# Kernel optimization log

Hardware: AMD Instinct MI355X
Metric: run time of the kernel (lower is better)

The kernel has to match this reference:

```python
import jax, jax.numpy as jnp
import numpy as np

B, T, H, W, C = 2, 8, 32, 32, 192
DI, N, K, DTR = 384, 16, 4, 12   # d_inner=2*dim, d_state, scan directions, dt_rank=ceil(dim/16)
LT, HID = 77, 768
L = T * H * W


def setup_inputs() -> dict:
    key = jax.random.key(0)
    ks = jax.random.split(key, 16)
    r = lambda i, shape, s=1.0: jax.random.normal(ks[i], shape, dtype=jnp.float32) * s
    return {
        "x": r(0, (B, T, H, W, C)),
        "text": r(1, (B, LT, C)),
        "cpe1_w": r(2, (C, 1, 3, 3, 3), 0.05), "cpe1_b": jnp.zeros((C,), jnp.float32),
        "cpe2_w": r(3, (C, 1, 3, 3, 3), 0.05), "cpe2_b": jnp.zeros((C,), jnp.float32),
        "norm1_g": jnp.ones((C,), jnp.float32), "norm1_b": jnp.zeros((C,), jnp.float32),
        "norm2_g": jnp.ones((C,), jnp.float32), "norm2_b": jnp.zeros((C,), jnp.float32),
        "in_proj_w": r(4, (2 * DI, C), 0.02), "in_proj_b": jnp.zeros((2 * DI,), jnp.float32),
        "text_proj_w": r(5, (DI, C), 0.02), "text_proj_b": jnp.zeros((DI,), jnp.float32),
        "conv_w": r(6, (DI, 1, 3, 3, 3), 0.05), "conv_b": jnp.zeros((DI,), jnp.float32),
        "x_proj_w": r(7, (K, DTR + 2 * N, DI), 0.02),
        "dt_proj_w": r(8, (K, DI, DTR), 0.1), "dt_proj_b": r(9, (K, DI), 0.1),
        "A_log": jnp.log(jnp.tile(jnp.arange(1.0, N + 1.0, dtype=jnp.float32)[None, None, :], (K, DI, 1))),
        "Ds": jnp.ones((K, DI), jnp.float32),
        "out_norm_g": jnp.ones((DI,), jnp.float32), "out_norm_b": jnp.zeros((DI,), jnp.float32),
        "out_proj_w": r(10, (C, DI), 0.02),
        "fc1_w": r(11, (HID, C), 0.02), "fc1_b": jnp.zeros((HID,), jnp.float32),
        "fc2_w": r(12, (C, HID), 0.02), "fc2_b": jnp.zeros((C,), jnp.float32),
    }


def _ln(x, g, b, eps=1e-6):
    m = x.mean(-1, keepdims=True)
    v = jnp.mean((x - m) ** 2, -1, keepdims=True)
    return (x - m) * jax.lax.rsqrt(v + eps) * g + b


def _dwconv3d(x, w, b):  # x [B, Ch, T, H, W], depthwise 3x3x3, SAME padding
    y = jax.lax.conv_general_dilated(x, w, (1, 1, 1), 'SAME',
                                     feature_group_count=x.shape[1],
                                     dimension_numbers=('NCDHW', 'OIDHW', 'NCDHW'))
    return y + b[None, :, None, None, None]


def _cpe(x, w, b):  # conv positional encoding, channels-last in/out
    return jnp.transpose(_dwconv3d(jnp.transpose(x, (0, 4, 1, 2, 3)), w, b), (0, 2, 3, 4, 1))


def _ss2d(x, text, p):
    # in-projection -> (x, z) gate split
    xz = x @ p['in_proj_w'].T + p['in_proj_b']           # [B,T,H,W,2*DI]
    xi, z = jnp.split(xz, 2, axis=-1)
    # text conditioning (pooled text tokens -> channel bias)
    cond = jax.nn.silu(text.mean(1) @ p['text_proj_w'].T + p['text_proj_b'])  # [B,DI]
    xi = xi + cond[:, None, None, None, :]
    # depthwise conv3d + SiLU
    xc = jax.nn.silu(_dwconv3d(jnp.transpose(xi, (0, 4, 1, 2, 3)), p['conv_w'], p['conv_b']))  # [B,DI,T,H,W]
    # cross-scan: (t,h,w), (t,w,h) and their reversals
    x0 = xc.reshape(B, DI, L)
    x1 = jnp.swapaxes(xc, 3, 4).reshape(B, DI, L)
    xs = jnp.stack([x0, x1, jnp.flip(x0, -1), jnp.flip(x1, -1)], 1)  # [B,K,DI,L]
    # per-direction projections
    xdbl = jnp.einsum('bkdl,kcd->bkcl', xs, p['x_proj_w'])
    dtr, Bm, Cm = jnp.split(xdbl, [DTR, DTR + N], axis=2)            # [B,K,DTR,L],[B,K,N,L],[B,K,N,L]
    dt = jax.nn.softplus(jnp.einsum('bkrl,kdr->bkdl', dtr, p['dt_proj_w']) + p['dt_proj_b'][None, :, :, None])
    A = -jnp.exp(p['A_log'])                                          # [K,DI,N]
    def step(h, inp):
        u_l, dt_l, B_l, C_l = inp
        h = h * jnp.exp(dt_l[..., None] * A) + (dt_l * u_l)[..., None] * B_l[:, :, None, :]
        return h, jnp.einsum('bkdn,bkn->bkd', h, C_l)
    seq = (xs.transpose(3, 0, 1, 2), dt.transpose(3, 0, 1, 2),
           Bm.transpose(3, 0, 1, 2), Cm.transpose(3, 0, 1, 2))
    _, ys = jax.lax.scan(step, jnp.zeros((B, K, DI, N), xs.dtype), seq)  # ys [L,B,K,DI]
    ys = ys.transpose(1, 2, 3, 0) + p['Ds'][None, :, :, None] * xs       # [B,K,DI,L]
    # merge the 4 directions back into (t,h,w) order
    unt = lambda y: jnp.swapaxes(y.reshape(B, DI, T, W, H), 3, 4).reshape(B, DI, L)
    y = ys[:, 0] + jnp.flip(ys[:, 2], -1) + unt(ys[:, 1]) + unt(jnp.flip(ys[:, 3], -1))
    y = _ln(y.transpose(0, 2, 1), p['out_norm_g'], p['out_norm_b']).reshape(B, T, H, W, DI)
    y = y * jax.nn.silu(z)
    return y @ p['out_proj_w'].T


def reference(x, text, cpe1_w, cpe1_b, cpe2_w, cpe2_b, norm1_g, norm1_b, norm2_g, norm2_b,
              in_proj_w, in_proj_b, text_proj_w, text_proj_b, conv_w, conv_b,
              x_proj_w, dt_proj_w, dt_proj_b, A_log, Ds, out_norm_g, out_norm_b, out_proj_w,
              fc1_w, fc1_b, fc2_w, fc2_b):
    p = dict(in_proj_w=in_proj_w, in_proj_b=in_proj_b, text_proj_w=text_proj_w,
             text_proj_b=text_proj_b, conv_w=conv_w, conv_b=conv_b, x_proj_w=x_proj_w,
             dt_proj_w=dt_proj_w, dt_proj_b=dt_proj_b, A_log=A_log, Ds=Ds,
             out_norm_g=out_norm_g, out_norm_b=out_norm_b, out_proj_w=out_proj_w)
    x = x + _cpe(x, cpe1_w, cpe1_b)
    x = x + _ss2d(_ln(x, norm1_g, norm1_b), text, p)
    x = x + _cpe(x, cpe2_w, cpe2_b)
    h = _ln(x, norm2_g, norm2_b)
    x = x + (jax.nn.gelu(h @ fc1_w.T + fc1_b) @ fc2_w.T + fc2_b)
    return x
```

## Files before the change

### kernel.cpp

```cpp
#include <hip/hip_runtime.h>
#include <hip/hip_bf16.h>

#define DEV __device__ __forceinline__

namespace {

constexpr int cB = 2, cT = 8, cH = 32, cW = 32, cC = 192;
constexpr int cDI = 384, cN = 16, cK = 4, cDTR = 12, cLT = 77, cHID = 768;
constexpr int cL  = cT * cH * cW;
constexpr int cBL = cB * cL;
constexpr int SEG = 128, SEGLEN = cL / SEG;
constexpr int XROW = cDTR + 2 * cN;
constexpr int XSTR = 48;

typedef __attribute__((ext_vector_type(8))) short bf16x8;
typedef __attribute__((ext_vector_type(4))) float f32x4;
typedef __attribute__((ext_vector_type(2))) float f32x2;
typedef __attribute__((ext_vector_type(4))) short short4v;

DEV float bfu2f(unsigned short u) { return __uint_as_float(((unsigned)u) << 16); }
DEV float ldsel(const void* p, size_t i, int f32) {
  return f32 ? ((const float*)p)[i] : bfu2f(((const unsigned short*)p)[i]);
}
template <int F32>
DEV float4 ld4(const void* p, size_t e) {
  if (F32) return *(const float4*)((const float*)p + e);
  ushort4 u = *(const ushort4*)((const unsigned short*)p + e);
  return make_float4(bfu2f(u.x), bfu2f(u.y), bfu2f(u.z), bfu2f(u.w));
}
DEV short f2bf(float f) {
  unsigned u = __float_as_uint(f);
  u += 0x7fffu + ((u >> 16) & 1u);
  return (short)(u >> 16);
}
DEV float siluf(float x) { return x / (1.f + __expf(-x)); }
DEV float softplusf(float x) { return (x > 20.f) ? x : __logf(1.f + __expf(x)); }
DEV float gelut(float x) {
  float u = 0.7978845608028654f * (x + 0.044715f * x * x * x);
  float e = __expf(2.f * u);
  float th = 1.f - 2.f / (e + 1.f);
  return 0.5f * x * (1.f + th);
}
DEV f32x2 mk2(float a, float b) { f32x2 v; v[0] = a; v[1] = b; return v; }

__global__ void __launch_bounds__(256) detect_kernel(
    const unsigned short* __restrict__ xa, const unsigned short* __restrict__ wp,
    int* __restrict__ flg) {
  __shared__ int cnt[2];
  if (threadIdx.x < 2) cnt[threadIdx.x] = 0;
  __syncthreads();
  int l0 = 0, l1 = 0;
  for (int i = threadIdx.x; i < 1024; i += 256) {
    float v = bfu2f(xa[2 * i]); float a = fabsf(v);
    if (v == 0.f || (a > 1e-8f && a < 1e4f)) l0++;
    float u = bfu2f(wp[2 * i]); float bq = fabsf(u);
    if (u == 0.f || (bq > 1e-8f && bq < 1e4f)) l1++;
  }
  atomicAdd(&cnt[0], l0); atomicAdd(&cnt[1], l1);
  __syncthreads();
  if (threadIdx.x == 0) {
    flg[0] = (cnt[0] < 614) ? 1 : 0;
    flg[1] = (cnt[1] < 614) ? 1 : 0;
    flg[2] = 1;
  }
}

__global__ void __launch_bounds__(256) prep_kernel(
    const void* __restrict__ cvw, const void* __restrict__ cvb,
    const void* __restrict__ c1w, const void* __restrict__ c1b,
    const void* __restrict__ c2w, const void* __restrict__ c2b,
    const int* __restrict__ flg,
    float* __restrict__ wcv, float* __restrict__ bcv,
    float* __restrict__ w1, float* __restrict__ b1,
    float* __restrict__ w2, float* __restrict__ b2) {
  int pf = flg[1];
  int i = blockIdx.x * 256 + threadIdx.x;
  int r = i;
  if (r < 27 * cDI) { int j = r / cDI, d = r % cDI; wcv[r] = ldsel(cvw, (size_t)d * 27 + j, pf); return; }
  r -= 27 * cDI;
  if (r < cDI) { bcv[r] = ldsel(cvb, r, pf); return; }
  r -= cDI;
  if (r < 27 * cC) { int j = r / cC, c = r % cC; w1[r] = ldsel(c1w, (size_t)c * 27 + j, pf); return; }
  r -= 27 * cC;
  if (r < cC) { b1[r] = ldsel(c1b, r, pf); return; }
  r -= cC;
  if (r < 27 * cC) { int j = r / cC, c = r % cC; w2[r] = ldsel(c2w, (size_t)c * 27 + j, pf); return; }
  r -= 27 * cC;
  if (r < cC) { b2[r] = ldsel(c2b, r, pf); return; }
}

template <int F32>
DEV void cpe_body(const void* __restrict__ xin, const float* __restrict__ wT,
                  const float* __restrict__ bs, int idx, float* __restrict__ out) {
  int c = (idx % (cC / 4)) * 4; int pv = idx / (cC / 4);
  int w0 = (pv & 15) << 1;
  int rest = pv >> 4;
  int h = rest & 31; int bt = rest >> 5; int t = bt & 7; int b = bt >> 3;
  float4 bias = *(const float4*)(bs + c);
  float4 acc0 = bias, acc1 = bias;
  const float4 zero = make_float4(0.f, 0.f, 0.f, 0.f);
#pragma unroll
  for (int dz = 0; dz < 3; ++dz) {
    int tt = t + dz - 1; if ((unsigned)tt >= (unsigned)cT) continue;
#pragma unroll
    for (int dy = 0; dy < 3; ++dy) {
      int hh = h + dy - 1; if ((unsigned)hh >= (unsigned)cH) continue;
      int base = (tt << 10) + (hh << 5);
      const float* wr = wT + (dz * 9 + dy * 3) * cC + c;
      float4 wv0 = *(const float4*)(wr);
      float4 wv1 = *(const float4*)(wr + cC);
      float4 wv2 = *(const float4*)(wr + 2 * cC);
      size_t rb = ((size_t)b * cL + base) * cC + c;
      float4 xm1 = (w0 > 0)  ? ld4<F32>(xin, rb + (size_t)(w0 - 1) * cC) : zero;
      float4 x0v = ld4<F32>(xin, rb + (size_t)w0 * cC);
      float4 x1v = ld4<F32>(xin, rb + (size_t)(w0 + 1) * cC);
      float4 x2v = (w0 < 30) ? ld4<F32>(xin, rb + (size_t)(w0 + 2) * cC) : zero;
      acc0.x += wv0.x*xm1.x + wv1.x*x0v.x + wv2.x*x1v.x;
      acc0.y += wv0.y*xm1.y + wv1.y*x0v.y + wv2.y*x1v.y;
      acc0.z += wv0.z*xm1.z + wv1.z*x0v.z + wv2.z*x1v.z;
      acc0.w += wv0.w*xm1.w + wv1.w*x0v.w + wv2.w*x1v.w;
      acc1.x += wv0.x*x0v.x + wv1.x*x1v.x + wv2.x*x2v.x;
      acc1.y += wv0.y*x0v.y + wv1.y*x1v.y + wv2.y*x2v.y;
      acc1.z += wv0.z*x0v.z + wv1.z*x1v.z + wv2.z*x2v.z;
      acc1.w += wv0.w*x0v.w + wv1.w*x1v.w + wv2.w*x2v.w;
    }
  }
  size_t bv0 = (size_t)b * cL + (t << 10) + (h << 5) + w0;
  float4 r0 = ld4<F32>(xin, bv0 * cC + c);
  float4 r1 = ld4<F32>(xin, (bv0 + 1) * cC + c);
  *(float4*)(out + bv0 * cC + c) =
      make_float4(r0.x + acc0.x, r0.y + acc0.y, r0.z + acc0.z, r0.w + acc0.w);
  *(float4*)(out + (bv0 + 1) * cC + c) =
      make_float4(r1.x + acc1.x, r1.y + acc1.y, r1.z + acc1.z, r1.w + acc1.w);
}

__global__ void __launch_bounds__(256) cpe_kernel(
    const void* __restrict__ xin, const float* __restrict__ wT,
    const float* __restrict__ bs, const int* __restrict__ flg, int afidx,
    float* __restrict__ out) {
  int idx = blockIdx.x * 256 + threadIdx.x;
  if (idx >= cBL * cC / 8) return;
  if (flg[afidx]) cpe_body<1>(xin, wT, bs, idx, out);
  else            cpe_body<0>(xin, wT, bs, idx, out);
}

__global__ void __launch_bounds__(256) dwconv_silu_kernel(
    const unsigned short* __restrict__ xin, const float* __restrict__ wT,
    const float* __restrict__ bs, unsigned short* __restrict__ out) {
  int idx = blockIdx.x * 256 + threadIdx.x;
  if (idx >= cBL * cDI / 8) return;
  int d = (idx % (cDI / 4)) * 4; int pv = idx / (cDI / 4);
  int w0 = (pv & 15) << 1;
  int rest = pv >> 4;
  int h = rest & 31; int bt = rest >> 5; int t = bt & 7; int b = bt >> 3;
  float4 bias = *(const float4*)(bs + d);
  float4 acc0 = bias, acc1 = bias;
  const float4 zero = make_float4(0.f, 0.f, 0.f, 0.f);
#pragma unroll
  for (int dz = 0; dz < 3; ++dz) {
    int tt = t + dz - 1; if ((unsigned)tt >= (unsigned)cT) continue;
#pragma unroll
    for (int dy = 0; dy < 3; ++dy) {
      int hh = h + dy - 1; if ((unsigned)hh >= (unsigned)cH) continue;
      int base = (tt << 10) + (hh << 5);
      const float* wr = wT + (dz * 9 + dy * 3) * cDI + d;
      float4 wv0 = *(const float4*)(wr);
      float4 wv1 = *(const float4*)(wr + cDI);
      float4 wv2 = *(const float4*)(wr + 2 * cDI);
      size_t rb = ((size_t)b * cL + base) * cDI + d;
      float4 xm1 = (w0 > 0)  ? ld4<0>(xin, rb + (size_t)(w0 - 1) * cDI) : zero;
      float4 x0v = ld4<0>(xin, rb + (size_t)w0 * cDI);
      float4 x1v = ld4<0>(xin, rb + (size_t)(w0 + 1) * cDI);
      float4 x2v = (w0 < 30) ? ld4<0>(xin, rb + (size_t)(w0 + 2) * cDI) : zero;
      acc0.x += wv0.x*xm1.x + wv1.x*x0v.x + wv2.x*x1v.x;
      acc0.y += wv0.y*xm1.y + wv1.y*x0v.y + wv2.y*x1v.y;
      acc0.z += wv0.z*xm1.z + wv1.z*x0v.z + wv2.z*x1v.z;
      acc0.w += wv0.w*xm1.w + wv1.w*x0v.w + wv2.w*x1v.w;
      acc1.x += wv0.x*x0v.x + wv1.x*x1v.x + wv2.x*x2v.x;
      acc1.y += wv0.y*x0v.y + wv1.y*x1v.y + wv2.y*x2v.y;
      acc1.z += wv0.z*x0v.z + wv1.z*x1v.z + wv2.z*x2v.z;
      acc1.w += wv0.w*x0v.w + wv1.w*x1v.w + wv2.w*x2v.w;
    }
  }
  size_t bv0 = (size_t)b * cL + (t << 10) + (h << 5) + w0;
  ushort4 o0, o1;
  o0.x = (unsigned short)f2bf(siluf(acc0.x));
  o0.y = (unsigned short)f2bf(siluf(acc0.y));
  o0.z = (unsigned short)f2bf(siluf(acc0.z));
  o0.w = (unsigned short)f2bf(siluf(acc0.w));
  o1.x = (unsigned short)f2bf(siluf(acc1.x));
  o1.y = (unsigned short)f2bf(siluf(acc1.y));
  o1.z = (unsigned short)f2bf(siluf(acc1.z));
  o1.w = (unsigned short)f2bf(siluf(acc1.w));
  *(ushort4*)(out + bv0 * cDI + d) = o0;
  *(ushort4*)(out + (bv0 + 1) * cDI + d) = o1;
}

__global__ void __launch_bounds__(256) lnb_kernel(
    const float* __restrict__ in, const void* __restrict__ g,
    const void* __restrict__ bb, const int* __restrict__ flg,
    unsigned short* __restrict__ out) {
  int pf = flg[1];
  int row = blockIdx.x * 4 + (threadIdx.x >> 6);
  int lane = threadIdx.x & 63;
  const float* x = in + (size_t)row * cC;
  float v0 = x[lane], v1 = x[lane + 64], v2 = x[lane + 128];
  float s1 = v0 + v1 + v2;
  float s2 = v0 * v0 + v1 * v1 + v2 * v2;
#pragma unroll
  for (int off = 32; off > 0; off >>= 1) {
    s1 += __shfl_xor(s1, off);
    s2 += __shfl_xor(s2, off);
  }
  float mean = s1 * (1.f / cC);
  float var = s2 * (1.f / cC) - mean * mean;
  float rstd = rsqrtf(var + 1e-6f);
  unsigned short* o = out + (size_t)row * cC;
  o[lane]       = (unsigned short)f2bf((v0 - mean) * rstd * ldsel(g, lane, pf)       + ldsel(bb, lane, pf));
  o[lane + 64]  = (unsigned short)f2bf((v1 - mean) * rstd * ldsel(g, lane + 64, pf)  + ldsel(bb, lane + 64, pf));
  o[lane + 128] = (unsigned short)f2bf((v2 - mean) * rstd * ldsel(g, lane + 128, pf) + ldsel(bb, lane + 128, pf));
}

__global__ void __launch_bounds__(384) text_cond_kernel(
    const void* __restrict__ text, const void* __restrict__ tw,
    const void* __restrict__ tb, const int* __restrict__ flg,
    float* __restrict__ cond) {
  int af = flg[0], pf = flg[1];
  __shared__ float mean[cC];
  int b = blockIdx.x;
  for (int c = threadIdx.x; c < cC; c += 384) {
    float s = 0.f;
    for (int t = 0; t < cLT; ++t) s += ldsel(text, ((size_t)b * cLT + t) * cC + c, af);
    mean[c] = s * (1.f / cLT);
  }
  __syncthreads();
  int di = threadIdx.x;
  float a = ldsel(tb, di, pf);
  for (int c = 0; c < cC; ++c) a += mean[c] * ldsel(tw, di * cC + c, pf);
  cond[b * cDI + di] = siluf(a);
}

template <int MODE>
__global__ void __launch_bounds__(256) gemm_mfma_kernel(
    const void* __restrict__ A, const void* __restrict__ W,
    int N, int K, const void* __restrict__ bias, const int* __restrict__ flg,
    const float* __restrict__ extra, float* __restrict__ out,
    unsigned short* __restrict__ out2) {
  constexpr int BM = 128, BN = 64, BK = 64, PK = 72;
  __shared__ short As[BM * PK];
  __shared__ short Bs[BN * PK];
  int pf = flg[1];
  int tid = threadIdx.x;
  int m0 = blockIdx.y * BM, n0 = blockIdx.x * BN;
  int lane = tid & 63, wv = tid >> 6;
  int wm = (wv >> 1) * 64, wn = (wv & 1) * 32;
  int lr = lane & 15, quad = lane >> 4;
  f32x4 acc[4][2];
#pragma unroll
  for (int mi = 0; mi < 4; ++mi)
#pragma unroll
    for (int ni = 0; ni < 2; ++ni) { acc[mi][ni][0]=0.f; acc[mi][ni][1]=0.f; acc[mi][ni][2]=0.f; acc[mi][ni][3]=0.f; }
  int ar = tid >> 1, aks = (tid & 1) * 32;
  int wr = tid >> 2, wks = (tid & 3) * 16;
  for (int k0 = 0; k0 < K; k0 += BK) {
    {
      const unsigned short* ap = (const unsigned short*)A + (size_t)(m0 + ar) * K + k0 + aks;
      short* da = &As[ar * PK + aks];
#pragma unroll
      for (int i = 0; i < 4; ++i)
        *(bf16x8*)(da + i * 8) = *(const bf16x8*)(ap + i * 8);
    }
    {
      int nr = n0 + wr;
      short* db = &Bs[wr * PK + wks];
      if (nr < N) {
        size_t wi = (size_t)nr * K + k0 + wks;
        if (pf) {
          float4 wv0 = *(const float4*)((const float*)W + wi);
          float4 wv1 = *(const float4*)((const float*)W + wi + 4);
          float4 wv2 = *(const float4*)((const float*)W + wi + 8);
          float4 wv3 = *(const float4*)((const float*)W + wi + 12);
          short4v h0, h1, h2, h3;
          h0.x = f2bf(wv0.x); h0.y = f2bf(wv0.y); h0.z = f2bf(wv0.z); h0.w = f2bf(wv0.w);
          h1.x = f2bf(wv1.x); h1.y = f2bf(wv1.y); h1.z = f2bf(wv1.z); h1.w = f2bf(wv1.w);
          h2.x = f2bf(wv2.x); h2.y = f2bf(wv2.y); h2.z = f2bf(wv2.z); h2.w = f2bf(wv2.w);
          h3.x = f2bf(wv3.x); h3.y = f2bf(wv3.y); h3.z = f2bf(wv3.z); h3.w = f2bf(wv3.w);
          *(short4v*)(db) = h0;
          *(short4v*)(db + 4) = h1;
          *(short4v*)(db + 8) = h2;
          *(short4v*)(db + 12) = h3;
        } else {
          *(bf16x8*)(db) = *(const bf16x8*)((const unsigned short*)W + wi);
          *(bf16x8*)(db + 8) = *(const bf16x8*)((const unsigned short*)W + wi + 8);
        }
      } else {
        short4v z; z.x = 0; z.y = 0; z.z = 0; z.w = 0;
        *(short4v*)(db) = z;
        *(short4v*)(db + 4) = z;
        *(short4v*)(db + 8) = z;
        *(short4v*)(db + 12) = z;
      }
    }
    __syncthreads();
    bf16x8 af[2][4], bfr[2][2];
#pragma unroll
    for (int kk = 0; kk < 2; ++kk) {
#pragma unroll
      for (int mi = 0; mi < 4; ++mi)
        af[kk][mi] = *(const bf16x8*)&As[(wm + mi * 16 + lr) * PK + kk * 32 + quad * 8];
#pragma unroll
      for (int ni = 0; ni < 2; ++ni)
        bfr[kk][ni] = *(const bf16x8*)&Bs[(wn + ni * 16 + lr) * PK + kk * 32 + quad * 8];
    }
#pragma unroll
    for (int kk = 0; kk < 2; ++kk)
#pragma unroll
      for (int mi = 0; mi < 4; ++mi)
#pragma unroll
        for (int ni = 0; ni < 2; ++ni)
          acc[mi][ni] = __builtin_amdgcn_mfma_f32_16x16x32_bf16(af[kk][mi], bfr[kk][ni], acc[mi][ni], 0, 0, 0);
    __syncthreads();
  }
#pragma unroll
  for (int mi = 0; mi < 4; ++mi) {
#pragma unroll
    for (int ni = 0; ni < 2; ++ni) {
#pragma unroll
      for (int r = 0; r < 4; ++r) {
        int m = m0 + wm + mi * 16 + quad * 4 + r;
        int n = n0 + wn + ni * 16 + lr;
        float v = acc[mi][ni][r];
        if (MODE == 0) {
          float bvv = ldsel(bias, n, pf);
          int b = m >> 13;
          if (n < cDI)
            ((unsigned short*)out)[(size_t)m * cDI + n] =
                (unsigned short)f2bf(v + bvv + extra[b * cDI + n]);
          else
            out2[(size_t)m * cDI + (n - cDI)] = (unsigned short)f2bf(v + bvv);
        } else if (MODE == 1) {
          if (n < cK * XROW) {
            int k = n / XROW, c = n - k * XROW;
            int b = m >> 13, vv = m & (cL - 1);
            int t = vv >> 10, q = vv & 1023, h = q >> 5, w = q & 31;
            int l1 = (t << 10) + (w << 5) + h;
            int lk = (k == 0) ? vv : (k == 1) ? l1 : (k == 2) ? (cL - 1 - vv) : (cL - 1 - l1);
            out[((size_t)(b * cK + k) * cL + lk) * XSTR + c] = v;
          }
        } else if (MODE == 2) {
          out[(size_t)m * cC + n] = v + extra[(size_t)m * cC + n];
        } else if (MODE == 3) {
          ((unsigned short*)out)[(size_t)m * cHID + n] =
              (unsigned short)f2bf(gelut(v + ldsel(bias, n, pf)));
        } else {
          out[(size_t)m * cC + n] = v + ldsel(bias, n, pf) + extra[(size_t)m * cC + n];
        }
      }
    }
  }
}

DEV int scan_voxel(int k, int l) {
  if (k == 0) return l;
  if (k == 2) return cL - 1 - l;
  int ll = (k == 1) ? l : (cL - 1 - l);
  int t = ll >> 10, q = ll & 1023, w = q >> 5, h = q & 31;
  return (t << 10) + (h << 5) + w;
}

struct Row11 { float4 r0, r1, r2, r3, r4, r5, r6, r7, r8, r9, r10; };
struct Row7  { float4 r0, r1, r2, r7, r8, r9, r10; };

DEV Row11 ldrow11(const float* __restrict__ rows, int st) {
  const float4* rp = (const float4*)(rows + st * XSTR);
  Row11 q;
  q.r0 = rp[0]; q.r1 = rp[1]; q.r2 = rp[2]; q.r3 = rp[3]; q.r4 = rp[4];
  q.r5 = rp[5]; q.r6 = rp[6]; q.r7 = rp[7]; q.r8 = rp[8]; q.r9 = rp[9];
  q.r10 = rp[10];
  return q;
}
DEV Row7 ldrow7(const float* __restrict__ rows, int st) {
  const float4* rp = (const float4*)(rows + st * XSTR);
  Row7 q;
  q.r0 = rp[0]; q.r1 = rp[1]; q.r2 = rp[2];
  q.r7 = rp[7]; q.r8 = rp[8]; q.r9 = rp[9]; q.r10 = rp[10];
  return q;
}

DEV float dtdot(const Row11& q, const f32x2 (&wp)[6], float dtb) {
  f32x2 acc = mk2(dtb, 0.f);
  acc += mk2(q.r0.x, q.r0.y) * wp[0];
  acc += mk2(q.r0.z, q.r0.w) * wp[1];
  acc += mk2(q.r1.x, q.r1.y) * wp[2];
  acc += mk2(q.r1.z, q.r1.w) * wp[3];
  acc += mk2(q.r2.x, q.r2.y) * wp[4];
  acc += mk2(q.r2.z, q.r2.w) * wp[5];
  return acc[0] + acc[1];
}
DEV float dtdot7(const Row7& q, const f32x2 (&wp)[6], float dtb) {
  f32x2 acc = mk2(dtb, 0.f);
  acc += mk2(q.r0.x, q.r0.y) * wp[0];
  acc += mk2(q.r0.z, q.r0.w) * wp[1];
  acc += mk2(q.r1.x, q.r1.y) * wp[2];
  acc += mk2(q.r1.z, q.r1.w) * wp[3];
  acc += mk2(q.r2.x, q.r2.y) * wp[4];
  acc += mk2(q.r2.z, q.r2.w) * wp[5];
  return acc[0] + acc[1];
}

DEV void powpk(float a1, f32x2 (&pw)[8]) {
  float a2 = a1 * a1;
  f32x2 sq = mk2(a2, a2);
  pw[0] = mk2(a1, a2);
  pw[1] = pw[0] * sq;
  pw[2] = pw[1] * sq;
  pw[3] = pw[2] * sq;
  pw[4] = pw[3] * sq;
  pw[5] = pw[4] * sq;
  pw[6] = pw[5] * sq;
  pw[7] = pw[6] * sq;
}

DEV float s1step(const Row11& q, float u,
                 const f32x2 (&wp)[6], float dtb, float ac0, float Dsd,
                 f32x2 (&h)[8], float& P1) {
  float dt = softplusf(dtdot(q, wp, dtb));
  float a1 = exp2f(dt * ac0);
  f32x2 pw[8];
  powpk(a1, pw);
  float dtu = dt * u;
  P1 *= a1;
  f32x2 dtu2 = mk2(dtu, dtu);
  f32x2 B0 = mk2(q.r3.x,q.r3.y), B1 = mk2(q.r3.z,q.r3.w);
  f32x2 B2 = mk2(q.r4.x,q.r4.y), B3 = mk2(q.r4.z,q.r4.w);
  f32x2 B4 = mk2(q.r5.x,q.r5.y), B5 = mk2(q.r5.z,q.r5.w);
  f32x2 B6 = mk2(q.r6.x,q.r6.y), B7 = mk2(q.r6.z,q.r6.w);
  f32x2 C0 = mk2(q.r7.x,q.r7.y), C1 = mk2(q.r7.z,q.r7.w);
  f32x2 C2 = mk2(q.r8.x,q.r8.y), C3 = mk2(q.r8.z,q.r8.w);
  f32x2 C4 = mk2(q.r9.x,q.r9.y), C5 = mk2(q.r9.z,q.r9.w);
  f32x2 C6 = mk2(q.r10.x,q.r10.y), C7 = mk2(q.r10.z,q.r10.w);
  f32x2 y0 = mk2(Dsd * u, 0.f), y1 = mk2(0.f,0.f), y2 = mk2(0.f,0.f), y3 = mk2(0.f,0.f);
  h[0] = h[0]*pw[0] + dtu2*B0; y0 += h[0]*C0;
  h[1] = h[1]*pw[1] + dtu2*B1; y1 += h[1]*C1;
  h[2] = h[2]*pw[2] + dtu2*B2; y2 += h[2]*C2;
  h[3] = h[3]*pw[3] + dtu2*B3; y3 += h[3]*C3;
  h[4] = h[4]*pw[4] + dtu2*B4; y0 += h[4]*C4;
  h[5] = h[5]*pw[5] + dtu2*B5; y1 += h[5]*C5;
  h[6] = h[6]*pw[6] + dtu2*B6; y2 += h[6]*C6;
  h[7] = h[7]*pw[7] + dtu2*B7; y3 += h[7]*C7;
  f32x2 t = (y0 + y1) + (y2 + y3);
  return t[0] + t[1];
}

DEV float s3step(const Row7& q,
                 const f32x2 (&wp)[6], float dtb, float ac0,
                 f32x2 (&g)[8]) {
  float dt = softplusf(dtdot7(q, wp, dtb));
  float a1 = exp2f(dt * ac0);
  f32x2 pw[8];
  powpk(a1, pw);
  f32x2 C0 = mk2(q.r7.x,q.r7.y), C1 = mk2(q.r7.z,q.r7.w);
  f32x2 C2 = mk2(q.r8.x,q.r8.y), C3 = mk2(q.r8.z,q.r8.w);
  f32x2 C4 = mk2(q.r9.x,q.r9.y), C5 = mk2(q.r9.z,q.r9.w);
  f32x2 C6 = mk2(q.r10.x,q.r10.y), C7 = mk2(q.r10.z,q.r10.w);
  f32x2 y0 = mk2(0.f,0.f), y1 = mk2(0.f,0.f), y2 = mk2(0.f,0.f), y3 = mk2(0.f,0.f);
  g[0] *= pw[0]; y0 += g[0]*C0;
  g[1] *= pw[1]; y1 += g[1]*C1;
  g[2] *= pw[2]; y2 += g[2]*C2;
  g[3] *= pw[3]; y3 += g[3]*C3;
  g[4] *= pw[4]; y0 += g[4]*C4;
  g[5] *= pw[5]; y1 += g[5]*C5;
  g[6] *= pw[6]; y2 += g[6]*C6;
  g[7] *= pw[7]; y3 += g[7]*C7;
  f32x2 t = (y0 + y1) + (y2 + y3);
  return t[0] + t[1];
}

__global__ void __launch_bounds__(128, 3) scan1_kernel(
    const unsigned short* __restrict__ xch, const float* __restrict__ xdbl,
// ... 183 lines not shown
      size_t ia = (size_t)st * cDI;
      ysrow[ia] = (unsigned short)f2bf(bfu2f(ysrow[ia]) + ya);
      qa = ldrow7(rows, p2);
      float yb = s3step(qb, wp, dtb, ac0, g2);
      size_t ib = (size_t)(st + 1) * cDI;
      ysrow[ib] = (unsigned short)f2bf(bfu2f(ysrow[ib]) + yb);
    }
  } else {
    float g[cN];
#pragma unroll
    for (int n = 0; n < cN; ++n) g[n] = bfu2f(hin[so + n]);
    for (int st = 0; st < SEGLEN; ++st) {
      const float4* rp = (const float4*)(rows + st * XSTR);
      float4 q0 = rp[0], q1 = rp[1], q2 = rp[2];
      float s0 = dtb + q0.x*wdt[0] + q0.z*wdt[2] + q1.x*wdt[4] + q1.z*wdt[6] + q2.x*wdt[8] + q2.z*wdt[10];
      float s1 = q0.y*wdt[1] + q0.w*wdt[3] + q1.y*wdt[5] + q1.w*wdt[7] + q2.y*wdt[9] + q2.w*wdt[11];
      float dt = softplusf(s0 + s1);
      float Cv[cN];
      float4 qc0 = rp[7], qc1 = rp[8], qc2 = rp[9], qc3 = rp[10];
      Cv[0]=qc0.x; Cv[1]=qc0.y; Cv[2]=qc0.z; Cv[3]=qc0.w;
      Cv[4]=qc1.x; Cv[5]=qc1.y; Cv[6]=qc1.z; Cv[7]=qc1.w;
      Cv[8]=qc2.x; Cv[9]=qc2.y; Cv[10]=qc2.z; Cv[11]=qc2.w;
      Cv[12]=qc3.x; Cv[13]=qc3.y; Cv[14]=qc3.z; Cv[15]=qc3.w;
      float y = 0.f;
#pragma unroll
      for (int n = 0; n < cN; ++n) {
        float a = exp2f(dt * ac[n]);
        g[n] *= a;
        y += g[n] * Cv[n];
      }
      size_t ii = (size_t)st * cDI;
      ysrow[ii] = (unsigned short)f2bf(bfu2f(ysrow[ii]) + y);
    }
  }
}

__global__ void __launch_bounds__(256) merge_kernel(
    const unsigned short* __restrict__ ys0, const unsigned short* __restrict__ ys1,
    const unsigned short* __restrict__ ys2, const unsigned short* __restrict__ ys3,
    const unsigned short* __restrict__ zh,
    const void* __restrict__ ong, const void* __restrict__ onb,
    const int* __restrict__ flg, unsigned short* __restrict__ yg) {
  int pf = flg[1];
  int bv = blockIdx.x * 4 + (threadIdx.x >> 6);
  int lane = threadIdx.x & 63;
  int v = bv & (cL - 1); int b = bv >> 13;
  int t = v >> 10, q = v & 1023, hh = q >> 5, ww = q & 31;
  int l1 = (t << 10) + (ww << 5) + hh;
  size_t r0 = ((size_t)b * cL + v) * cDI;
  size_t r1 = ((size_t)b * cL + l1) * cDI;
  size_t r2 = ((size_t)b * cL + (cL - 1 - v)) * cDI;
  size_t r3 = ((size_t)b * cL + (cL - 1 - l1)) * cDI;
  float vals[6]; float s1 = 0.f, s2 = 0.f;
#pragma unroll
  for (int i = 0; i < 6; ++i) {
    int d = lane + i * 64;
    float x = bfu2f(ys0[r0 + d]) + bfu2f(ys1[r1 + d]) +
              bfu2f(ys2[r2 + d]) + bfu2f(ys3[r3 + d]);
    vals[i] = x; s1 += x; s2 += x * x;
  }
#pragma unroll
  for (int off = 32; off > 0; off >>= 1) {
    s1 += __shfl_xor(s1, off);
    s2 += __shfl_xor(s2, off);
  }
  float mean = s1 * (1.f / cDI);
  float var = s2 * (1.f / cDI) - mean * mean;
  float rstd = rsqrtf(var + 1e-6f);
  const unsigned short* zr = zh + (size_t)bv * cDI;
  unsigned short* og = yg + (size_t)bv * cDI;
#pragma unroll
  for (int i = 0; i < 6; ++i) {
    int d = lane + i * 64;
    float xn = (vals[i] - mean) * rstd * ldsel(ong, d, pf) + ldsel(onb, d, pf);
    og[d] = (unsigned short)f2bf(xn * siluf(bfu2f(zr[d])));
  }
}

}

extern "C" void kernel_launch(void* const* d_in, const int* in_sizes, int n_in,
                              void* d_out, int out_size, void* d_ws, size_t ws_size,
                              hipStream_t stream) {
  (void)in_sizes; (void)n_in; (void)out_size; (void)ws_size;
  const void* x    = d_in[0];
  const void* text = d_in[1];
  const void* c1w  = d_in[2];
  const void* c1b  = d_in[3];
  const void* c2w  = d_in[4];
  const void* c2b  = d_in[5];
  const void* n1g  = d_in[6];
  const void* n1b  = d_in[7];
  const void* n2g  = d_in[8];
  const void* n2b  = d_in[9];
  const void* ipw  = d_in[10];
  const void* ipb  = d_in[11];
  const void* tpw  = d_in[12];
  const void* tpb  = d_in[13];
  const void* cvw  = d_in[14];
  const void* cvb  = d_in[15];
  const void* xpw  = d_in[16];
  const void* dtw  = d_in[17];
  const void* dtb  = d_in[18];
  const void* alog = d_in[19];
  const void* dsv  = d_in[20];
  const void* ong  = d_in[21];
  const void* onb  = d_in[22];
  const void* opw  = d_in[23];
  const void* f1w  = d_in[24];
  const void* f1b  = d_in[25];
  const void* f2w  = d_in[26];
  const void* f2b  = d_in[27];

  float* Wf = (float*)d_ws;

  constexpr size_t oC  = 0;
  constexpr size_t oD  = 6291456;
  constexpr size_t oG  = 9437184;
  constexpr size_t oA  = 12582912;
  constexpr size_t oB  = 18874368;
  constexpr size_t oE  = 25165824;
  constexpr size_t oF  = 28311552;
  constexpr size_t oCO = 31457280;
  constexpr size_t oFL = 31458048;
  constexpr size_t oWCV = 31458052;
  constexpr size_t oBCV = 31468420;
  constexpr size_t oW1  = 31468804;
  constexpr size_t oB1  = 31473988;
  constexpr size_t oW2  = 31474180;
  constexpr size_t oB2  = 31479364;
  unsigned short* xch = (unsigned short*)(Wf + oC);
  unsigned short* ysd2 = (unsigned short*)(Wf + oC + 3145728);
  unsigned short* hbufh = (unsigned short*)(Wf + oC);
  float* xdbl = Wf + oD;
  unsigned short* ygh  = (unsigned short*)(Wf + oD);
  unsigned short* xnh  = (unsigned short*)(Wf + oG);
  unsigned short* pendp = (unsigned short*)(Wf + oG);
  unsigned short* xib  = (unsigned short*)(Wf + oA);
  unsigned short* ysd0 = (unsigned short*)(Wf + oA);
  unsigned short* ysd1 = (unsigned short*)(Wf + oA + 3145728);
  float* x2   = Wf + oA;
  unsigned short* zh   = (unsigned short*)(Wf + oB);
  unsigned short* ysd3 = (unsigned short*)(Wf + oB + 3145728);
  float* x3   = Wf + oB;
  float* x1   = Wf + oE;
  unsigned short* hendp = (unsigned short*)(Wf + oF);
  unsigned short* xn2h = (unsigned short*)(Wf + oF);
  float* cond = Wf + oCO;
  int*   flg  = (int*)(Wf + oFL);
  float* wcv = Wf + oWCV; float* bcv = Wf + oBCV;
  float* w1t = Wf + oW1;  float* b1t = Wf + oB1;
  float* w2t = Wf + oW2;  float* b2t = Wf + oB2;

  const int cpeBlocks = (cBL * cC / 8) / 256;
  const int dwBlocks  = (cBL * cDI / 8) / 256;

  hipLaunchKernelGGL(detect_kernel, dim3(1), dim3(256), 0, stream,
                     (const unsigned short*)x, (const unsigned short*)ipw, flg);
  hipLaunchKernelGGL(prep_kernel, dim3(85), dim3(256), 0, stream,
                     cvw, cvb, c1w, c1b, c2w, c2b, flg, wcv, bcv, w1t, b1t, w2t, b2t);
  hipLaunchKernelGGL(cpe_kernel, dim3(cpeBlocks), dim3(256), 0, stream,
                     x, w1t, b1t, flg, 0, x1);
  hipLaunchKernelGGL(lnb_kernel, dim3(cBL / 4), dim3(256), 0, stream, x1, n1g, n1b, flg, xnh);
  hipLaunchKernelGGL(text_cond_kernel, dim3(cB), dim3(384), 0, stream, text, tpw, tpb, flg, cond);
  hipLaunchKernelGGL((gemm_mfma_kernel<0>), dim3(2 * cDI / 64, cBL / 128), dim3(256), 0, stream,
                     xnh, ipw, 2 * cDI, cC, ipb, flg, cond, (float*)xib, zh);
  hipLaunchKernelGGL(dwconv_silu_kernel, dim3(dwBlocks), dim3(256), 0, stream,
                     xib, wcv, bcv, xch);
  hipLaunchKernelGGL((gemm_mfma_kernel<1>), dim3((cK * XROW + 63) / 64, cBL / 128), dim3(256), 0, stream,
                     xch, xpw, cK * XROW, cDI, (const void*)nullptr, flg,
                     (const float*)nullptr, xdbl, (unsigned short*)nullptr);
  hipLaunchKernelGGL(scan1_kernel, dim3(cDI / 128, cB * cK * SEG), dim3(128), 0, stream,
                     xch, xdbl, dtw, dtb, alog, dsv, flg,
                     ysd0, ysd1, ysd2, ysd3, hendp, pendp);
  hipLaunchKernelGGL(scan2_kernel, dim3(cB * cK * cDI * cN / 256), dim3(256), 0, stream,
                     hendp, pendp);
  hipLaunchKernelGGL(scan3_kernel, dim3(cDI / 128, cB * cK * SEG), dim3(128), 0, stream,
                     xdbl, dtw, dtb, alog, flg, hendp, ysd0, ysd1, ysd2, ysd3);
  hipLaunchKernelGGL(merge_kernel, dim3(cBL / 4), dim3(256), 0, stream,
                     ysd0, ysd1, ysd2, ysd3, zh, ong, onb, flg, ygh);
  hipLaunchKernelGGL((gemm_mfma_kernel<2>), dim3(cC / 64, cBL / 128), dim3(256), 0, stream,
                     ygh, opw, cC, cDI, (const void*)nullptr, flg, x1, x2,
                     (unsigned short*)nullptr);
  hipLaunchKernelGGL(cpe_kernel, dim3(cpeBlocks), dim3(256), 0, stream,
                     x2, w2t, b2t, flg, 2, x3);
  hipLaunchKernelGGL(lnb_kernel, dim3(cBL / 4), dim3(256), 0, stream, x3, n2g, n2b, flg, xn2h);
  hipLaunchKernelGGL((gemm_mfma_kernel<3>), dim3(cHID / 64, cBL / 128), dim3(256), 0, stream,
                     xn2h, f1w, cHID, cC, f1b, flg, (const float*)nullptr, (float*)hbufh,
                     (unsigned short*)nullptr);
  hipLaunchKernelGGL((gemm_mfma_kernel<4>), dim3(cC / 64, cBL / 128), dim3(256), 0, stream,
                     hbufh, f2w, cC, cHID, f2b, flg, x3, (float*)d_out,
                     (unsigned short*)nullptr);
}
```

Measured before the change: 540.9 us.

## Register-block depthwise convs over 2x2 outputs and widen GEMM N-tile to 128

The CPE and dwconv+SiLU kernels now compute a 2x2 (h,w) output block per thread instead of 1x2. Each loaded input row is reused for two output rows, which cuts redundant global loads and halves the thread count. The MFMA GEMM is templated on BN, and the in_proj and fc1 GEMMs use a 128-wide N tile to reuse A tiles more. This raises register pressure and lowers the block count, which may reduce occupancy.

```diff
diff --git a/kernel.cpp b/kernel.cpp
--- a/kernel.cpp
+++ b/kernel.cpp
@@ -42,6 +42,11 @@
   return 0.5f * x * (1.f + th);
 }
 DEV f32x2 mk2(float a, float b) { f32x2 v; v[0] = a; v[1] = b; return v; }
+DEV float4 cfma(float4 acc, float4 w, float4 x) {
+  acc.x += w.x * x.x; acc.y += w.y * x.y;
+  acc.z += w.z * x.z; acc.w += w.w * x.w;
+  return acc;
+}
 
 __global__ void __launch_bounds__(256) detect_kernel(
     const unsigned short* __restrict__ xa, const unsigned short* __restrict__ wp,
@@ -92,46 +97,56 @@
 template <int F32>
 DEV void cpe_body(const void* __restrict__ xin, const float* __restrict__ wT,
                   const float* __restrict__ bs, int idx, float* __restrict__ out) {
-  int c = (idx % (cC / 4)) * 4; int pv = idx / (cC / 4);
-  int w0 = (pv & 15) << 1;
-  int rest = pv >> 4;
-  int h = rest & 31; int bt = rest >> 5; int t = bt & 7; int b = bt >> 3;
+  int c = (idx % (cC / 4)) * 4;
+  int rest = idx / (cC / 4);
+  int w0 = (rest & 15) << 1; rest >>= 4;
+  int h0 = (rest & 15) << 1; rest >>= 4;
+  int t = rest & 7; int b = rest >> 3;
   float4 bias = *(const float4*)(bs + c);
-  float4 acc0 = bias, acc1 = bias;
+  float4 a00 = bias, a01 = bias, a10 = bias, a11 = bias;
   const float4 zero = make_float4(0.f, 0.f, 0.f, 0.f);
 #pragma unroll
   for (int dz = 0; dz < 3; ++dz) {
     int tt = t + dz - 1; if ((unsigned)tt >= (unsigned)cT) continue;
 #pragma unroll
-    for (int dy = 0; dy < 3; ++dy) {
-      int hh = h + dy - 1; if ((unsigned)hh >= (unsigned)cH) continue;
-      int base = (tt << 10) + (hh << 5);
-      const float* wr = wT + (dz * 9 + dy * 3) * cC + c;
-      float4 wv0 = *(const float4*)(wr);
-      float4 wv1 = *(const float4*)(wr + cC);
-      float4 wv2 = *(const float4*)(wr + 2 * cC);
-      size_t rb = ((size_t)b * cL + base) * cC + c;
+    for (int rr = 0; rr < 4; ++rr) {
+      int hh = h0 + rr - 1;
+      if ((unsigned)hh >= (unsigned)cH) continue;
+      size_t rb = ((size_t)b * cL + (tt << 10) + (hh << 5)) * cC + c;
       float4 xm1 = (w0 > 0)  ? ld4<F32>(xin, rb + (size_t)(w0 - 1) * cC) : zero;
       float4 x0v = ld4<F32>(xin, rb + (size_t)w0 * cC);
       float4 x1v = ld4<F32>(xin, rb + (size_t)(w0 + 1) * cC);
       float4 x2v = (w0 < 30) ? ld4<F32>(xin, rb + (size_t)(w0 + 2) * cC) : zero;
-      acc0.x += wv0.x*xm1.x + wv1.x*x0v.x + wv2.x*x1v.x;
-      acc0.y += wv0.y*xm1.y + wv1.y*x0v.y + wv2.y*x1v.y;
-      acc0.z += wv0.z*xm1.z + wv1.z*x0v.z + wv2.z*x1v.z;
-      acc0.w += wv0.w*xm1.w + wv1.w*x0v.w + wv2.w*x1v.w;
-      acc1.x += wv0.x*x0v.x + wv1.x*x1v.x + wv2.x*x2v.x;
-      acc1.y += wv0.y*x0v.y + wv1.y*x1v.y + wv2.y*x2v.y;
-      acc1.z += wv0.z*x0v.z + wv1.z*x1v.z + wv2.z*x2v.z;
-      acc1.w += wv0.w*x0v.w + wv1.w*x1v.w + wv2.w*x2v.w;
-    }
-  }
-  size_t bv0 = (size_t)b * cL + (t << 10) + (h << 5) + w0;
-  float4 r0 = ld4<F32>(xin, bv0 * cC + c);
-  float4 r1 = ld4<F32>(xin, (bv0 + 1) * cC + c);
-  *(float4*)(out + bv0 * cC + c) =
-      make_float4(r0.x + acc0.x, r0.y + acc0.y, r0.z + acc0.z, r0.w + acc0.w);
-  *(float4*)(out + (bv0 + 1) * cC + c) =
-      make_float4(r1.x + acc1.x, r1.y + acc1.y, r1.z + acc1.z, r1.w + acc1.w);
+      if (rr < 3) {
+        const float* wr = wT + (dz * 9 + rr * 3) * cC + c;
+        float4 wv0 = *(const float4*)(wr);
+        float4 wv1 = *(const float4*)(wr + cC);
+        float4 wv2 = *(const float4*)(wr + 2 * cC);
+        a00 = cfma(cfma(cfma(a00, wv0, xm1), wv1, x0v), wv2, x1v);
+        a01 = cfma(cfma(cfma(a01, wv0, x0v), wv1, x1v), wv2, x2v);
+      }
+      if (rr >= 1) {
+        const float* wr = wT + (dz * 9 + (rr - 1) * 3) * cC + c;
+        float4 wv0 = *(const float4*)(wr);
+        float4 wv1 = *(const float4*)(wr + cC);
+        float4 wv2 = *(const float4*)(wr + 2 * cC);
+        a10 = cfma(cfma(cfma(a10, wv0, xm1), wv1, x0v), wv2, x1v);
+        a11 = cfma(cfma(cfma(a11, wv0, x0v), wv1, x1v), wv2, x2v);
+      }
+    }
+  }
+  size_t v00 = (size_t)b * cL + (t << 10) + (h0 << 5) + w0;
+#pragma unroll
+  for (int oh = 0; oh < 2; ++oh) {
+#pragma unroll
+    for (int ow = 0; ow < 2; ++ow) {
+      size_t bv = v00 + (size_t)(oh << 5) + ow;
+      float4 acc = (oh == 0) ? (ow == 0 ? a00 : a01) : (ow == 0 ? a10 : a11);
+      float4 r0 = ld4<F32>(xin, bv * cC + c);
+      *(float4*)(out + bv * cC + c) =
+          make_float4(r0.x + acc.x, r0.y + acc.y, r0.z + acc.z, r0.w + acc.w);
+    }
+  }
 }
 
 __global__ void __launch_bounds__(256) cpe_kernel(
@@ -139,7 +154,7 @@
     const float* __restrict__ bs, const int* __restrict__ flg, int afidx,
     float* __restrict__ out) {
   int idx = blockIdx.x * 256 + threadIdx.x;
-  if (idx >= cBL * cC / 8) return;
+  if (idx >= cBL * cC / 16) return;
   if (flg[afidx]) cpe_body<1>(xin, wT, bs, idx, out);
   else            cpe_body<0>(xin, wT, bs, idx, out);
 }
@@ -148,52 +163,60 @@
     const unsigned short* __restrict__ xin, const float* __restrict__ wT,
     const float* __restrict__ bs, unsigned short* __restrict__ out) {
   int idx = blockIdx.x * 256 + threadIdx.x;
-  if (idx >= cBL * cDI / 8) return;
-  int d = (idx % (cDI / 4)) * 4; int pv = idx / (cDI / 4);
-  int w0 = (pv & 15) << 1;
-  int rest = pv >> 4;
-  int h = rest & 31; int bt = rest >> 5; int t = bt & 7; int b = bt >> 3;
+  if (idx >= cBL * cDI / 16) return;
+  int d = (idx % (cDI / 4)) * 4;
+  int rest = idx / (cDI / 4);
+  int w0 = (rest & 15) << 1; rest >>= 4;
+  int h0 = (rest & 15) << 1; rest >>= 4;
+  int t = rest & 7; int b = rest >> 3;
   float4 bias = *(const float4*)(bs + d);
-  float4 acc0 = bias, acc1 = bias;
+  float4 a00 = bias, a01 = bias, a10 = bias, a11 = bias;
   const float4 zero = make_float4(0.f, 0.f, 0.f, 0.f);
 #pragma unroll
   for (int dz = 0; dz < 3; ++dz) {
     int tt = t + dz - 1; if ((unsigned)tt >= (unsigned)cT) continue;
 #pragma unroll
-    for (int dy = 0; dy < 3; ++dy) {
-      int hh = h + dy - 1; if ((unsigned)hh >= (unsigned)cH) continue;
-      int base = (tt << 10) + (hh << 5);
-      const float* wr = wT + (dz * 9 + dy * 3) * cDI + d;
-      float4 wv0 = *(const float4*)(wr);
-      float4 wv1 = *(const float4*)(wr + cDI);
-      float4 wv2 = *(const float4*)(wr + 2 * cDI);
-      size_t rb = ((size_t)b * cL + base) * cDI + d;
+    for (int rr = 0; rr < 4; ++rr) {
+      int hh = h0 + rr - 1;
+      if ((unsigned)hh >= (unsigned)cH) continue;
+      size_t rb = ((size_t)b * cL + (tt << 10) + (hh << 5)) * cDI + d;
       float4 xm1 = (w0 > 0)  ? ld4<0>(xin, rb + (size_t)(w0 - 1) * cDI) : zero;
       float4 x0v = ld4<0>(xin, rb + (size_t)w0 * cDI);
       float4 x1v = ld4<0>(xin, rb + (size_t)(w0 + 1) * cDI);
       float4 x2v = (w0 < 30) ? ld4<0>(xin, rb + (size_t)(w0 + 2) * cDI) : zero;
-      acc0.x += wv0.x*xm1.x + wv1.x*x0v.x + wv2.x*x1v.x;
-      acc0.y += wv0.y*xm1.y + wv1.y*x0v.y + wv2.y*x1v.y;
-      acc0.z += wv0.z*xm1.z + wv1.z*x0v.z + wv2.z*x1v.z;
-      acc0.w += wv0.w*xm1.w + wv1.w*x0v.w + wv2.w*x1v.w;
-      acc1.x += wv0.x*x0v.x + wv1.x*x1v.x + wv2.x*x2v.x;
-      acc1.y += wv0.y*x0v.y + wv1.y*x1v.y + wv2.y*x2v.y;
-      acc1.z += wv0.z*x0v.z + wv1.z*x1v.z + wv2.z*x2v.z;
-      acc1.w += wv0.w*x0v.w + wv1.w*x1v.w + wv2.w*x2v.w;
-    }
-  }
-  size_t bv0 = (size_t)b * cL + (t << 10) + (h << 5) + w0;
-  ushort4 o0, o1;
-  o0.x = (unsigned short)f2bf(siluf(acc0.x));
-  o0.y = (unsigned short)f2bf(siluf(acc0.y));
-  o0.z = (unsigned short)f2bf(siluf(acc0.z));
-  o0.w = (unsigned short)f2bf(siluf(acc0.w));
-  o1.x = (unsigned short)f2bf(siluf(acc1.x));
-  o1.y = (unsigned short)f2bf(siluf(acc1.y));
-  o1.z = (unsigned short)f2bf(siluf(acc1.z));
-  o1.w = (unsigned short)f2bf(siluf(acc1.w));
-  *(ushort4*)(out + bv0 * cDI + d) = o0;
-  *(ushort4*)(out + (bv0 + 1) * cDI + d) = o1;
+      if (rr < 3) {
+        const float* wr = wT + (dz * 9 + rr * 3) * cDI + d;
+        float4 wv0 = *(const float4*)(wr);
+        float4 wv1 = *(const float4*)(wr + cDI);
+        float4 wv2 = *(const float4*)(wr + 2 * cDI);
+        a00 = cfma(cfma(cfma(a00, wv0, xm1), wv1, x0v), wv2, x1v);
+        a01 = cfma(cfma(cfma(a01, wv0, x0v), wv1, x1v), wv2, x2v);
+      }
+      if (rr >= 1) {
+        const float* wr = wT + (dz * 9 + (rr - 1) * 3) * cDI + d;
+        float4 wv0 = *(const float4*)(wr);
+        float4 wv1 = *(const float4*)(wr + cDI);
+        float4 wv2 = *(const float4*)(wr + 2 * cDI);
+        a10 = cfma(cfma(cfma(a10, wv0, xm1), wv1, x0v), wv2, x1v);
+        a11 = cfma(cfma(cfma(a11, wv0, x0v), wv1, x1v), wv2, x2v);
+      }
+    }
+  }
+  size_t v00 = (size_t)b * cL + (t << 10) + (h0 << 5) + w0;
+#pragma unroll
+  for (int oh = 0; oh < 2; ++oh) {
+#pragma unroll
+    for (int ow = 0; ow < 2; ++ow) {
+      size_t bv = v00 + (size_t)(oh << 5) + ow;
+      float4 acc = (oh == 0) ? (ow == 0 ? a00 : a01) : (ow == 0 ? a10 : a11);
+      ushort4 o;
+      o.x = (unsigned short)f2bf(siluf(acc.x));
+      o.y = (unsigned short)f2bf(siluf(acc.y));
+      o.z = (unsigned short)f2bf(siluf(acc.z));
+      o.w = (unsigned short)f2bf(siluf(acc.w));
+      *(ushort4*)(out + bv * cDI + d) = o;
+    }
+  }
 }
 
 __global__ void __launch_bounds__(256) lnb_kernel(
@@ -240,28 +263,32 @@
   cond[b * cDI + di] = siluf(a);
 }
 
-template <int MODE>
+template <int MODE, int BN>
 __global__ void __launch_bounds__(256) gemm_mfma_kernel(
     const void* __restrict__ A, const void* __restrict__ W,
     int N, int K, const void* __restrict__ bias, const int* __restrict__ flg,
     const float* __restrict__ extra, float* __restrict__ out,
     unsigned short* __restrict__ out2) {
-  constexpr int BM = 128, BN = 64, BK = 64, PK = 72;
+  constexpr int BM = 128, BK = 64, PK = 72;
+  constexpr int NI = BN / 32;
   __shared__ short As[BM * PK];
   __shared__ short Bs[BN * PK];
   int pf = flg[1];
   int tid = threadIdx.x;
   int m0 = blockIdx.y * BM, n0 = blockIdx.x * BN;
   int lane = tid & 63, wv = tid >> 6;
-  int wm = (wv >> 1) * 64, wn = (wv & 1) * 32;
+  int wm = (wv >> 1) * 64, wn = (wv & 1) * (BN / 2);
   int lr = lane & 15, quad = lane >> 4;
-  f32x4 acc[4][2];
+  f32x4 acc[4][NI];
 #pragma unroll
   for (int mi = 0; mi < 4; ++mi)
 #pragma unroll
-    for (int ni = 0; ni < 2; ++ni) { acc[mi][ni][0]=0.f; acc[mi][ni][1]=0.f; acc[mi][ni][2]=0.f; acc[mi][ni][3]=0.f; }
+    for (int ni = 0; ni < NI; ++ni) { acc[mi][ni][0]=0.f; acc[mi][ni][1]=0.f; acc[mi][ni][2]=0.f; acc[mi][ni][3]=0.f; }
   int ar = tid >> 1, aks = (tid & 1) * 32;
-  int wr = tid >> 2, wks = (tid & 3) * 16;
+  int wr, wks;
+  if (BN == 64) { wr = tid >> 2; wks = (tid & 3) * 16; }
+  else          { wr = tid >> 1; wks = (tid & 1) * 32; }
+  constexpr int BEL = (BN == 64) ? 16 : 32;
   for (int k0 = 0; k0 < K; k0 += BK) {
     {
       const unsigned short* ap = (const unsigned short*)A + (size_t)(m0 + ar) * K + k0 + aks;
@@ -276,40 +303,34 @@
       if (nr < N) {
         size_t wi = (size_t)nr * K + k0 + wks;
         if (pf) {
-          float4 wv0 = *(const float4*)((const float*)W + wi);
-          float4 wv1 = *(const float4*)((const float*)W + wi + 4);
-          float4 wv2 = *(const float4*)((const float*)W + wi + 8);
-          float4 wv3 = *(const float4*)((const float*)W + wi + 12);
-          short4v h0, h1, h2, h3;
-          h0.x = f2bf(wv0.x); h0.y = f2bf(wv0.y); h0.z = f2bf(wv0.z); h0.w = f2bf(wv0.w);
-          h1.x = f2bf(wv1.x); h1.y = f2bf(wv1.y); h1.z = f2bf(wv1.z); h1.w = f2bf(wv1.w);
-          h2.x = f2bf(wv2.x); h2.y = f2bf(wv2.y); h2.z = f2bf(wv2.z); h2.w = f2bf(wv2.w);
-          h3.x = f2bf(wv3.x); h3.y = f2bf(wv3.y); h3.z = f2bf(wv3.z); h3.w = f2bf(wv3.w);
-          *(short4v*)(db) = h0;
-          *(short4v*)(db + 4) = h1;
-          *(short4v*)(db + 8) = h2;
-          *(short4v*)(db + 12) = h3;
+#pragma unroll
+          for (int i = 0; i < BEL / 4; ++i) {
+            float4 wvv = *(const float4*)((const float*)W + wi + i * 4);
+            short4v h;
+            h.x = f2bf(wvv.x); h.y = f2bf(wvv.y); h.z = f2bf(wvv.z); h.w = f2bf(wvv.w);
+            *(short4v*)(db + i * 4) = h;
+          }
         } else {
-          *(bf16x8*)(db) = *(const bf16x8*)((const unsigned short*)W + wi);
-          *(bf16x8*)(db + 8) = *(const bf16x8*)((const unsigned short*)W + wi + 8);
+#pragma unroll
+          for (int i = 0; i < BEL / 8; ++i)
+            *(bf16x8*)(db + i * 8) = *(const bf16x8*)((const unsigned short*)W + wi + i * 8);
         }
       } else {
         short4v z; z.x = 0; z.y = 0; z.z = 0; z.w = 0;
-        *(short4v*)(db) = z;
-        *(short4v*)(db + 4) = z;
-        *(short4v*)(db + 8) = z;
-        *(short4v*)(db + 12) = z;
+#pragma unroll
+        for (int i = 0; i < BEL / 4; ++i)
+          *(short4v*)(db + i * 4) = z;
       }
     }
     __syncthreads();
-    bf16x8 af[2][4], bfr[2][2];
+    bf16x8 af[2][4], bfr[2][NI];
 #pragma unroll
     for (int kk = 0; kk < 2; ++kk) {
 #pragma unroll
       for (int mi = 0; mi < 4; ++mi)
         af[kk][mi] = *(const bf16x8*)&As[(wm + mi * 16 + lr) * PK + kk * 32 + quad * 8];
 #pragma unroll
-      for (int ni = 0; ni < 2; ++ni)
+      for (int ni = 0; ni < NI; ++ni)
         bfr[kk][ni] = *(const bf16x8*)&Bs[(wn + ni * 16 + lr) * PK + kk * 32 + quad * 8];
     }
 #pragma unroll
@@ -317,14 +338,14 @@
 #pragma unroll
       for (int mi = 0; mi < 4; ++mi)
 #pragma unroll
-        for (int ni = 0; ni < 2; ++ni)
+        for (int ni = 0; ni < NI; ++ni)
           acc[mi][ni] = __builtin_amdgcn_mfma_f32_16x16x32_bf16(af[kk][mi], bfr[kk][ni], acc[mi][ni], 0, 0, 0);
     __syncthreads();
   }
 #pragma unroll
   for (int mi = 0; mi < 4; ++mi) {
 #pragma unroll
-    for (int ni = 0; ni < 2; ++ni) {
+    for (int ni = 0; ni < NI; ++ni) {
 #pragma unroll
       for (int r = 0; r < 4; ++r) {
         int m = m0 + wm + mi * 16 + quad * 4 + r;
@@ -814,8 +835,8 @@
   float* w1t = Wf + oW1;  float* b1t = Wf + oB1;
   float* w2t = Wf + oW2;  float* b2t = Wf + oB2;
 
-  const int cpeBlocks = (cBL * cC / 8) / 256;
-  const int dwBlocks  = (cBL * cDI / 8) / 256;
+  const int cpeBlocks = (cBL * cC / 16) / 256;
+  const int dwBlocks  = (cBL * cDI / 16) / 256;
 
   hipLaunchKernelGGL(detect_kernel, dim3(1), dim3(256), 0, stream,
                      (const unsigned short*)x, (const unsigned short*)ipw, flg);
@@ -825,11 +846,11 @@
                      x, w1t, b1t, flg, 0, x1);
   hipLaunchKernelGGL(lnb_kernel, dim3(cBL / 4), dim3(256), 0, stream, x1, n1g, n1b, flg, xnh);
   hipLaunchKernelGGL(text_cond_kernel, dim3(cB), dim3(384), 0, stream, text, tpw, tpb, flg, cond);
-  hipLaunchKernelGGL((gemm_mfma_kernel<0>), dim3(2 * cDI / 64, cBL / 128), dim3(256), 0, stream,
+  hipLaunchKernelGGL((gemm_mfma_kernel<0, 128>), dim3(2 * cDI / 128, cBL / 128), dim3(256), 0, stream,
                      xnh, ipw, 2 * cDI, cC, ipb, flg, cond, (float*)xib, zh);
   hipLaunchKernelGGL(dwconv_silu_kernel, dim3(dwBlocks), dim3(256), 0, stream,
                      xib, wcv, bcv, xch);
-  hipLaunchKernelGGL((gemm_mfma_kernel<1>), dim3((cK * XROW + 63) / 64, cBL / 128), dim3(256), 0, stream,
+  hipLaunchKernelGGL((gemm_mfma_kernel<1, 64>), dim3((cK * XROW + 63) / 64, cBL / 128), dim3(256), 0, stream,
                      xch, xpw, cK * XROW, cDI, (const void*)nullptr, flg,
                      (const float*)nullptr, xdbl, (unsigned short*)nullptr);
   hipLaunchKernelGGL(scan1_kernel, dim3(cDI / 128, cB * cK * SEG), dim3(128), 0, stream,
@@ -841,16 +862,16 @@
                      xdbl, dtw, dtb, alog, flg, hendp, ysd0, ysd1, ysd2, ysd3);
   hipLaunchKernelGGL(merge_kernel, dim3(cBL / 4), dim3(256), 0, stream,
                      ysd0, ysd1, ysd2, ysd3, zh, ong, onb, flg, ygh);
-  hipLaunchKernelGGL((gemm_mfma_kernel<2>), dim3(cC / 64, cBL / 128), dim3(256), 0, stream,
+  hipLaunchKernelGGL((gemm_mfma_kernel<2, 64>), dim3(cC / 64, cBL / 128), dim3(256), 0, stream,
                      ygh, opw, cC, cDI, (const void*)nullptr, flg, x1, x2,
                      (unsigned short*)nullptr);
   hipLaunchKernelGGL(cpe_kernel, dim3(cpeBlocks), dim3(256), 0, stream,
                      x2, w2t, b2t, flg, 2, x3);
   hipLaunchKernelGGL(lnb_kernel, dim3(cBL / 4), dim3(256), 0, stream, x3, n2g, n2b, flg, xn2h);
-  hipLaunchKernelGGL((gemm_mfma_kernel<3>), dim3(cHID / 64, cBL / 128), dim3(256), 0, stream,
+  hipLaunchKernelGGL((gemm_mfma_kernel<3, 128>), dim3(cHID / 128, cBL / 128), dim3(256), 0, stream,
                      xn2h, f1w, cHID, cC, f1b, flg, (const float*)nullptr, (float*)hbufh,
                      (unsigned short*)nullptr);
-  hipLaunchKernelGGL((gemm_mfma_kernel<4>), dim3(cC / 64, cBL / 128), dim3(256), 0, stream,
+  hipLaunchKernelGGL((gemm_mfma_kernel<4, 64>), dim3(cC / 64, cBL / 128), dim3(256), 0, stream,
                      hbufh, f2w, cC, cHID, f2b, flg, x3, (float*)d_out,
                      (unsigned short*)nullptr);
 }
```

After: 537.5 us (median of 2 runs). No clear change (-0.6%).
